# Kernel optimization log

Measured on AMD Instinct MI355X. Metric: run time of the kernel, lower is better.

Reference implementation:

```python
import jax, jax.numpy as jnp
import numpy as np

B, S, D, H = 2, 2048, 2048, 16
HD = D // H  # head_dim = 128
ROPE_BASE = 10000.0


def _rope_interleaved(x, cos, sin):
    # x: [B, S, H, HD]; cos/sin: [S, HD//2]
    xe = x[..., 0::2]
    xo = x[..., 1::2]
    c = cos[None, :, None, :]
    s = sin[None, :, None, :]
    oe = xe * c - xo * s
    oo = xe * s + xo * c
    # re-interleave pairs back to last dim
    return jnp.stack([oe, oo], axis=-1).reshape(x.shape)


def setup_inputs() -> dict:
    key = jax.random.key(0)
    k0, k1, k2, k3 = jax.random.split(key, 4)
    scale = D ** -0.5
    x = jax.random.normal(k0, (B, S, D), dtype=jnp.float32)
    wqk = jax.random.normal(k1, (2 * D, D), dtype=jnp.float32) * scale
    wv = jax.random.normal(k2, (D, D), dtype=jnp.float32) * scale
    wo = jax.random.normal(k3, (D, D), dtype=jnp.float32) * scale
    return {"x": x, "wqk": wqk, "wv": wv, "wo": wo}


def reference(x, wqk, wv, wo):
    b, s, d = x.shape
    # fused QK projection -> [B, S, 2, H, HD]
    xqk = (x @ wqk.T).reshape(b, s, 2, H, HD)
    xq = xqk[:, :, 0]
    xk = xqk[:, :, 1]
    xv = (x @ wv.T).reshape(b, s, H, HD)

    # interleaved rotary embedding (seqlen_offset=0, no-cache path)
    inv_freq = 1.0 / (ROPE_BASE ** (jnp.arange(0, HD, 2, dtype=jnp.float32) / HD))
    freqs = jnp.arange(s, dtype=jnp.float32)[:, None] * inv_freq[None, :]  # [S, HD//2]
    cos, sin = jnp.cos(freqs), jnp.sin(freqs)
    xq = _rope_interleaved(xq, cos, sin)
    xk = _rope_interleaved(xk, cos, sin)

    # causal scaled-dot-product attention
    scores = jnp.einsum("bqhd,bkhd->bhqk", xq, xk) * (HD ** -0.5)
    causal = jnp.tril(jnp.ones((s, s), dtype=bool))
    scores = jnp.where(causal[None, None], scores, jnp.finfo(scores.dtype).min)
    probs = jax.nn.softmax(scores, axis=-1)
    out = jnp.einsum("bhqk,bkhd->bqhd", probs, xv).reshape(b, s, d)
    return out @ wo.T
```

## Files before the change

kernel.cpp:

```cpp
#include <hip/hip_runtime.h>
#include <hip/hip_bf16.h>

#define NB 2
#define SEQ 2048
#define DMODEL 2048
#define NH 16
#define HD 128
#define QSCALE (0.08838834764831845f * 1.44269504088896f)
#define THRL2 11.5f

using bf16x8 = __attribute__((ext_vector_type(8))) __bf16;
using f32x4  = __attribute__((ext_vector_type(4))) float;

#define MFMA16 __builtin_amdgcn_mfma_f32_16x16x32_bf16

typedef __attribute__((address_space(1))) const void* gptr_t;
typedef __attribute__((address_space(3))) void* lptr_t;

__device__ inline void gload_lds16(const unsigned short* g, unsigned short* l) {
    __builtin_amdgcn_global_load_lds((gptr_t)g, (lptr_t)l, 16, 0, 0);
}

__device__ inline unsigned short f2b(float f) {
    unsigned u = __builtin_bit_cast(unsigned, f);
    u += 0x7FFF + ((u >> 16) & 1);
    return (unsigned short)(u >> 16);
}
__device__ inline float b2f(unsigned short h) {
    return __builtin_bit_cast(float, (unsigned)h << 16);
}
__device__ inline float fexp2(float x) {
    float r;
    asm("v_exp_f32 %0, %1" : "=v"(r) : "v"(x));
    return r;
}
__device__ inline unsigned cvtpk(float a, float b) {
    unsigned r;
    asm("v_cvt_pk_bf16_f32 %0, %1, %2" : "=v"(r) : "v"(a), "v"(b));
    return r;
}

__global__ void cast_all(const float* __restrict__ x, const float* __restrict__ wqk,
                         const float* __restrict__ wv, const float* __restrict__ wo,
                         unsigned short* __restrict__ xb, unsigned short* __restrict__ wb,
                         float2* __restrict__ tab) {
    int idx = blockIdx.x * 256 + threadIdx.x;
    if (idx < 6291456) {
        const float* src; unsigned short* dst; int off;
        if (idx < 2097152)      { src = x;   dst = xb;             off = 0; }
        else if (idx < 4194304) { src = wqk; dst = wb;             off = 2097152; }
        else if (idx < 5242880) { src = wv;  dst = wb + 8388608;   off = 4194304; }
        else                    { src = wo;  dst = wb + 12582912;  off = 5242880; }
        int i = (idx - off) * 4;
        float4 v = *reinterpret_cast<const float4*>(src + i);
        ushort4 o;
        o.x = f2b(v.x); o.y = f2b(v.y); o.z = f2b(v.z); o.w = f2b(v.w);
        *reinterpret_cast<ushort4*>(dst + i) = o;
    } else {
        int k = idx - 6291456;
        int i = k & 63;
        int s = k >> 6;
        float inv = exp2f(-13.287712379549449f * (float)i * (1.0f / 64.0f));
        float ang = (float)s * inv;
        float sn, cs;
        sincosf(ang, &sn, &cs);
        tab[k] = make_float2(cs, sn);
    }
}

template<int MODE>
__global__ __launch_bounds__(512) void gemm8p(const unsigned short* __restrict__ A,
                                              const unsigned short* __restrict__ Bw,
                                              void* __restrict__ Cout,
                                              unsigned short* __restrict__ qb,
                                              unsigned short* __restrict__ kbp,
                                              unsigned short* __restrict__ vx,
                                              const float2* __restrict__ tab,
                                              int M, int N, int K) {
    __shared__ __align__(16) char lds[98304];
    int tid = threadIdx.x;
    int lane = tid & 63;
    int wid = tid >> 6;
    int wm = wid >> 2, wn = wid & 3;
    int row0 = blockIdx.y * 128;
    int col0 = blockIdx.x * 256;
    int lr = lane & 15, g = lane >> 4;

    const unsigned short* srcA[2];
    const unsigned short* srcB[4];
#pragma unroll
    for (int i = 0; i < 2; i++) {
        int chunk = i * 512 + tid;
        int ksub = chunk >> 9;
        int cw = chunk & 511;
        int row = cw >> 2, c = cw & 3;
        int cs = c ^ ((row >> 1) & 3);
        srcA[i] = A + (size_t)(row0 + row) * K + ksub * 32 + cs * 8;
    }
#pragma unroll
    for (int i = 0; i < 4; i++) {
        int chunk = i * 512 + tid;
        int ksub = chunk >> 10;
        int cw = chunk & 1023;
        int row = cw >> 2, c = cw & 3;
        int cs = c ^ ((row >> 1) & 3);
        srcB[i] = Bw + (size_t)(col0 + row) * K + ksub * 32 + cs * 8;
    }

    int offA[4][2], offB[4][2];
#pragma unroll
    for (int i = 0; i < 4; i++) {
        int row = wm * 64 + i * 16 + lr;
#pragma unroll
        for (int ks = 0; ks < 2; ks++)
            offA[i][ks] = ks * 8192 + row * 64 + ((g ^ ((row >> 1) & 3)) * 16);
    }
#pragma unroll
    for (int j = 0; j < 4; j++) {
        int row = wn * 64 + j * 16 + lr;
#pragma unroll
        for (int ks = 0; ks < 2; ks++)
            offB[j][ks] = ks * 16384 + row * 64 + ((g ^ ((row >> 1) & 3)) * 16);
    }

    f32x4 acc[4][4] = {};
    int NT = K >> 6;

#define STAGE8(t) {                                                                   \
        int kb_ = (t) * 64;                                                           \
        int bs_ = ((t) & 1) * 49152;                                                  \
        _Pragma("unroll")                                                             \
        for (int i_ = 0; i_ < 2; i_++)                                                \
            gload_lds16(srcA[i_] + kb_,                                               \
                (unsigned short*)(lds + bs_ + (i_ * 512 + (tid & ~63)) * 16));        \
        _Pragma("unroll")                                                             \
        for (int i_ = 0; i_ < 4; i_++)                                                \
            gload_lds16(srcB[i_] + kb_,                                               \
                (unsigned short*)(lds + bs_ + 16384 + (i_ * 512 + (tid & ~63)) * 16)); \
    }

    STAGE8(0);
    for (int t = 0; t < NT; ++t) {
        if (t + 1 < NT) {
            STAGE8(t + 1);
            asm volatile("s_waitcnt vmcnt(6)" ::: "memory");
        } else {
            asm volatile("s_waitcnt vmcnt(0)" ::: "memory");
        }
        __builtin_amdgcn_s_barrier();
        __builtin_amdgcn_sched_barrier(0);

        const char* ab = lds + (t & 1) * 49152;
        const char* bb = ab + 16384;

        bf16x8 b[4][2], a[2][2];
#pragma unroll
        for (int j = 0; j < 4; j++)
#pragma unroll
            for (int ks = 0; ks < 2; ks++)
                b[j][ks] = *reinterpret_cast<const bf16x8*>(bb + offB[j][ks]);
#pragma unroll
        for (int i = 0; i < 2; i++)
#pragma unroll
            for (int ks = 0; ks < 2; ks++)
                a[i][ks] = *reinterpret_cast<const bf16x8*>(ab + offA[i][ks]);
        asm volatile("s_waitcnt lgkmcnt(0)" ::: "memory");
        __builtin_amdgcn_sched_barrier(0);
        __builtin_amdgcn_s_setprio(1);
#pragma unroll
        for (int ks = 0; ks < 2; ks++)
#pragma unroll
            for (int i = 0; i < 2; i++)
#pragma unroll
                for (int j = 0; j < 4; j++)
                    acc[i][j] = MFMA16(a[i][ks], b[j][ks], acc[i][j], 0, 0, 0);
        __builtin_amdgcn_s_setprio(0);

        bf16x8 a2[2][2];
#pragma unroll
        for (int i = 0; i < 2; i++)
#pragma unroll
            for (int ks = 0; ks < 2; ks++)
                a2[i][ks] = *reinterpret_cast<const bf16x8*>(ab + offA[2 + i][ks]);
        asm volatile("s_waitcnt lgkmcnt(0)" ::: "memory");
        __builtin_amdgcn_sched_barrier(0);
        __builtin_amdgcn_s_barrier();
        __builtin_amdgcn_sched_barrier(0);
        __builtin_amdgcn_s_setprio(1);
#pragma unroll
        for (int ks = 0; ks < 2; ks++)
#pragma unroll
            for (int i = 0; i < 2; i++)
#pragma unroll
                for (int j = 0; j < 4; j++)
                    acc[2 + i][j] = MFMA16(a2[i][ks], b[j][ks], acc[2 + i][j], 0, 0, 0);
        __builtin_amdgcn_s_setprio(0);
    }
#undef STAGE8

    int orow = g * 4;
    if (MODE == 0) {
#pragma unroll
        for (int i = 0; i < 4; i++) {
#pragma unroll
            for (int j = 0; j < 4; j++) {
                int r0 = row0 + wm * 64 + i * 16 + orow;
                int c  = col0 + wn * 64 + j * 16 + lr;
#pragma unroll
                for (int r = 0; r < 4; r++)
                    ((float*)Cout)[(size_t)(r0 + r) * N + c] = acc[i][j][r];
            }
        }
    } else {
        int bx = blockIdx.x;
        if (bx < 16) {
            const bool isQ = (bx < 8);
            unsigned short* dst = isQ ? qb : kbp;
#pragma unroll
            for (int i = 0; i < 4; i++) {
#pragma unroll
                for (int j = 0; j < 4; j++) {
                    int c = col0 + wn * 64 + j * 16 + lr;
                    int cc = c & 2047;
                    int h = cc >> 7, d = cc & 127, i2 = d >> 1;
                    int odd = lr & 1;
#pragma unroll
                    for (int r = 0; r < 4; r++) {
                        int trow = row0 + wm * 64 + i * 16 + orow + r;
                        int s = trow & (SEQ - 1), bb2 = trow >> 11;
                        float v = acc[i][j][r];
                        float pv = __shfl_xor(v, 1);
                        float2 cssn = tab[s * 64 + i2];
                        float out = odd ? (pv * cssn.y + v * cssn.x)
                                        : (v * cssn.x - pv * cssn.y);
                        if (isQ) out *= QSCALE;
                        dst[((size_t)((bb2 * NH + h) * SEQ + s)) * HD + d] = f2b(out);
                    }
                }
            }
        } else {
#pragma unroll
            for (int i = 0; i < 4; i++) {
#pragma unroll
                for (int j = 0; j < 4; j++) {
                    int cc = col0 + wn * 64 + j * 16 + lr - 4096;
#pragma unroll
                    for (int r = 0; r < 4; r++) {
                        int trow = row0 + wm * 64 + i * 16 + orow + r;
                        vx[(size_t)trow * 2048 + cc] = f2b(acc[i][j][r]);
                    }
                }
            }
        }
    }
}

__global__ __launch_bounds__(256) void v_tr(const unsigned short* __restrict__ vx,
                                            unsigned short* __restrict__ vt) {
    __shared__ unsigned short tl[64][68];
    int bid = blockIdx.x;
    int st = bid & 31;
    int dt = (bid >> 5) & 1;
    int bh = bid >> 6;
    int b = bh >> 4, h = bh & 15;
    int tid = threadIdx.x;
    int rr = tid >> 2;
    int rc = (tid & 3) * 16;

    const unsigned short* src = vx + (size_t)(b * SEQ + st * 64 + rr) * 2048 + h * HD + dt * 64 + rc;
    uint4 v0 = *reinterpret_cast<const uint4*>(src);
    uint4 v1 = *reinterpret_cast<const uint4*>(src + 8);
    *reinterpret_cast<uint4*>(&tl[rr][rc]) = v0;
    *reinterpret_cast<uint4*>(&tl[rr][rc + 8]) = v1;
    __syncthreads();

    unsigned short tmp[16];
#pragma unroll
    for (int k = 0; k < 16; k++) tmp[k] = tl[rc + k][rr];
    unsigned short* dst = vt + (size_t)(bh * HD + dt * 64 + rr) * SEQ + st * 64 + rc;
    *reinterpret_cast<uint4*>(dst)     = *reinterpret_cast<const uint4*>(&tmp[0]);
    *reinterpret_cast<uint4*>(dst + 8) = *reinterpret_cast<const uint4*>(&tmp[8]);
}

__global__ __launch_bounds__(64, 2) void attn8(const unsigned short* __restrict__ Q,
                                               const unsigned short* __restrict__ Kb,
                                               const unsigned short* __restrict__ Vt,
                                               unsigned short* __restrict__ O) {
    __shared__ __align__(16) char lds[18432];

    int lane = threadIdx.x;
    int bid = blockIdx.x;
    int qt = 63 - (bid >> 5);
    int bh = bid & 31;
    int q0 = qt * 32;
    int ktiles = qt + 1;
    int lr = lane & 15;
    int g  = lane >> 4;
    int g4 = g * 4;
    int lk = g * 8;

    const unsigned short* Qp = Q  + (size_t)bh * SEQ * HD;
    const unsigned short* Kp = Kb + (size_t)bh * SEQ * HD;
    const unsigned short* Vp = Vt + (size_t)bh * HD * SEQ;
    char* pl = lds + 16384;
    int b = bh >> 4;
    int h = bh & 15;

    int srcoff[8];
#pragma unroll
    for (int i2 = 0; i2 < 8; ++i2) {
        int r = i2 * 4 + g;
        srcoff[i2] = r * HD + ((lr ^ (r & 7)) * 8);
    }

#define STAGEK32(bufbase, kvbase)                                                   \
    {                                                                               \
        const unsigned short* kbase = Kp + (size_t)(kvbase) * HD;                   \
        _Pragma("unroll")                                                           \
        for (int i2 = 0; i2 < 8; ++i2)                                              \
            gload_lds16(kbase + srcoff[i2],                                         \
                        (unsigned short*)(lds + (bufbase) + i2 * 1024));            \
    }

    bf16x8 qf[2][4];
#pragma unroll
    for (int f = 0; f < 2; f++)
#pragma unroll
        for (int kb = 0; kb < 4; kb++)
            qf[f][kb] = *reinterpret_cast<const bf16x8*>(Qp + (size_t)(q0 + f * 16 + lr) * HD + kb * 32 + lk);

    f32x4 oacc[2][8] = {};
    float m[2] = { -1e30f, -1e30f }, l[2] = { 0.0f, 0.0f };
    int qrow[2] = { q0 + lr, q0 + 16 + lr };

    STAGEK32(0, 0);

    int cur = 0;
    for (int t = 0; t < ktiles; ++t) {
        int kv0 = t * 32;
        if (t + 1 < ktiles) {
            STAGEK32((cur ^ 1) * 8192, kv0 + 32);
            asm volatile("s_waitcnt vmcnt(8)" ::: "memory");
        } else {
            asm volatile("s_waitcnt vmcnt(0)" ::: "memory");
        }
        __builtin_amdgcn_sched_barrier(0);

        char* kb_c = lds + cur * 8192;
        f32x4 s[2][2] = {};
#pragma unroll
        for (int kb = 0; kb < 4; kb++) {
#pragma unroll
            for (int jj = 0; jj < 2; jj++) {
                int row = jj * 16 + lr;
                int cin = ((kb * 4 + g) ^ (row & 7));
                bf16x8 kf = *reinterpret_cast<const bf16x8*>(kb_c + row * 256 + cin * 16);
                s[0][jj] = MFMA16(kf, qf[0][kb], s[0][jj], 0, 0, 0);
                s[1][jj] = MFMA16(kf, qf[1][kb], s[1][jj], 0, 0, 0);
            }
        }

        bf16x8 vf[8];
#pragma unroll
        for (int db = 0; db < 8; db++)
            vf[db] = *reinterpret_cast<const bf16x8*>(Vp + (size_t)(db * 16 + lr) * SEQ + kv0 + lk);

#pragma unroll
        for (int f = 0; f < 2; f++) {
            int q = qrow[f];
            bool full = (kv0 + 31 <= q0 + f * 16);
            float mx = -1e30f;
            if (full) {
#pragma unroll
                for (int jj = 0; jj < 2; jj++)
#pragma unroll
                    for (int r = 0; r < 4; r++)
                        mx = fmaxf(mx, s[f][jj][r]);
            } else {
#pragma unroll
                for (int jj = 0; jj < 2; jj++)
#pragma unroll
                    for (int r = 0; r < 4; r++) {
                        int kv = kv0 + jj * 16 + g4 + r;
                        float v = (kv <= q) ? s[f][jj][r] : -1e30f;
                        s[f][jj][r] = v;
                        mx = fmaxf(mx, v);
                    }
            }
            mx = fmaxf(mx, __shfl_xor(mx, 16));
            mx = fmaxf(mx, __shfl_xor(mx, 32));

            if (!__all(mx <= m[f] + THRL2)) {
                float mn = fmaxf(m[f], mx);
                float sc = fexp2(m[f] - mn);
                m[f] = mn;
                l[f] *= sc;
#pragma unroll
                for (int db = 0; db < 8; db++)
#pragma unroll
                    for (int r = 0; r < 4; r++)
                        oacc[f][db][r] *= sc;
            }

            int row = f * 16 + lr;
            int rb = row * 64;
            int sw = (row & 3) << 4;
            float rs = 0.0f;
#pragma unroll
            for (int jj = 0; jj < 2; jj++)
#pragma unroll
                for (int hh = 0; hh < 2; hh++) {
                    float p0 = fexp2(s[f][jj][2 * hh]     - m[f]);
                    float p1 = fexp2(s[f][jj][2 * hh + 1] - m[f]);
                    rs += p0 + p1;
                    unsigned pk = cvtpk(p0, p1);
                    int colb = jj * 32 + g * 8 + 4 * hh;
                    *reinterpret_cast<unsigned*>(pl + rb + (colb ^ sw)) = pk;
                }
            rs += __shfl_xor(rs, 16);
            rs += __shfl_xor(rs, 32);
            l[f] += rs;
        }

        asm volatile("s_waitcnt lgkmcnt(0)" ::: "memory");
        __builtin_amdgcn_sched_barrier(0);

        bf16x8 pb[2];
#pragma unroll
        for (int f = 0; f < 2; f++) {
            int row = f * 16 + lr;
            int off = row * 64 + ((g * 16) ^ ((row & 3) << 4));
            pb[f] = *reinterpret_cast<const bf16x8*>(pl + off);
        }
#pragma unroll
        for (int db = 0; db < 8; db++) {
            oacc[0][db] = MFMA16(vf[db], pb[0], oacc[0][db], 0, 0, 0);
            oacc[1][db] = MFMA16(vf[db], pb[1], oacc[1][db], 0, 0, 0);
        }

        cur ^= 1;
    }

#pragma unroll
    for (int f = 0; f < 2; f++) {
        float inv = 1.0f / l[f];
        int q = q0 + f * 16 + lr;
        unsigned short* op = O + ((size_t)(b * SEQ + q)) * DMODEL + h * HD;
#pragma unroll
        for (int db = 0; db < 8; db++) {
            ushort4 o4;
            o4.x = f2b(oacc[f][db][0] * inv);
            o4.y = f2b(oacc[f][db][1] * inv);
            o4.z = f2b(oacc[f][db][2] * inv);
            o4.w = f2b(oacc[f][db][3] * inv);
            *reinterpret_cast<ushort4*>(op + db * 16 + g4) = o4;
        }
    }
#undef STAGEK32
}

extern "C" void kernel_launch(void* const* d_in, const int* in_sizes, int n_in,
                              void* d_out, int out_size, void* d_ws, size_t ws_size,
                              hipStream_t stream) {
    const float* x   = (const float*)d_in[0];
    const float* wqk = (const float*)d_in[1];
    const float* wv  = (const float*)d_in[2];
    const float* wo  = (const float*)d_in[3];

    unsigned short* xb  = (unsigned short*)d_ws;
    unsigned short* wb  = xb  + (size_t)8388608;
    unsigned short* qb  = wb  + (size_t)16777216;
    unsigned short* kb  = qb  + (size_t)8388608;
    unsigned short* vx  = kb  + (size_t)8388608;
    unsigned short* vt  = vx  + (size_t)8388608;
    unsigned short* ao  = vt  + (size_t)8388608;
    float2* tab = (float2*)(ao + (size_t)8388608);

    cast_all<<<25088, 256, 0, stream>>>(x, wqk, wv, wo, xb, wb, tab);

    gemm8p<2><<<dim3(24, 32), 512, 0, stream>>>(xb, wb, nullptr, qb, kb, vx, tab, 4096, 6144, 2048);

    v_tr<<<2048, 256, 0, stream>>>(vx, vt);

    attn8<<<2048, 64, 0, stream>>>(qb, kb, vt, ao);

    gemm8p<0><<<dim3(8, 32), 512, 0, stream>>>(ao, wb + 12582912, d_out, nullptr, nullptr, nullptr, nullptr, 4096, 2048, 2048);
}
```

Measured before the change: 279.5 us.

## Use 256x256-tile QKV GEMM and write V transposed directly from epilogue

Replaces the 128x256-tile QKV projection GEMM with a new 256x256-tile kernel that uses 128 KB of LDS, double-buffered with direct global-to-LDS loads, giving more operand reuse per tile. Its V epilogue writes the transposed bf16 layout directly, so the separate v_tr transpose kernel and the intermediate vx buffer are removed. The output projection GEMM is simplified to a non-templated version. The trade-offs are fewer blocks (384) across the GPU, which may cause wave-quantization or occupancy loss, and less coalesced strided ushort4 stores for V.

```diff
diff --git a/kernel.cpp b/kernel.cpp
--- a/kernel.cpp
+++ b/kernel.cpp
@@ -68,14 +68,188 @@
     }
 }
 
-template<int MODE>
+__global__ __launch_bounds__(512) void gemm256(const unsigned short* __restrict__ A,
+                                               const unsigned short* __restrict__ Bw,
+                                               unsigned short* __restrict__ qb,
+                                               unsigned short* __restrict__ kbp,
+                                               unsigned short* __restrict__ vt,
+                                               const float2* __restrict__ tab,
+                                               int M, int N, int K) {
+    __shared__ __align__(16) char lds[131072];
+    int tid = threadIdx.x;
+    int lane = tid & 63;
+    int wid = tid >> 6;
+    int wm = wid >> 2, wn = wid & 3;
+    int row0 = blockIdx.y * 256;
+    int col0 = blockIdx.x * 256;
+    int lr = lane & 15, g = lane >> 4;
+
+    const unsigned short* srcA[4];
+    const unsigned short* srcB[4];
+#pragma unroll
+    for (int i = 0; i < 4; i++) {
+        int chunk = i * 512 + tid;
+        int ksub = chunk >> 10;
+        int cw = chunk & 1023;
+        int row = cw >> 2, c = cw & 3;
+        int cs = c ^ ((row >> 1) & 3);
+        srcA[i] = A  + (size_t)(row0 + row) * K + ksub * 32 + cs * 8;
+        srcB[i] = Bw + (size_t)(col0 + row) * K + ksub * 32 + cs * 8;
+    }
+
+    int offA[8][2], offB[4][2];
+#pragma unroll
+    for (int i = 0; i < 8; i++) {
+        int row = wm * 128 + i * 16 + lr;
+#pragma unroll
+        for (int ks = 0; ks < 2; ks++)
+            offA[i][ks] = ks * 16384 + row * 64 + ((g ^ ((row >> 1) & 3)) * 16);
+    }
+#pragma unroll
+    for (int j = 0; j < 4; j++) {
+        int row = wn * 64 + j * 16 + lr;
+#pragma unroll
+        for (int ks = 0; ks < 2; ks++)
+            offB[j][ks] = 32768 + ks * 16384 + row * 64 + ((g ^ ((row >> 1) & 3)) * 16);
+    }
+
+    f32x4 acc[8][4] = {};
+    int NT = K >> 6;
+
+#define STAGE256(t) {                                                                 \
+        int kb_ = (t) * 64;                                                           \
+        int bs_ = ((t) & 1) * 65536;                                                  \
+        _Pragma("unroll")                                                             \
+        for (int i_ = 0; i_ < 4; i_++)                                                \
+            gload_lds16(srcA[i_] + kb_,                                               \
+                (unsigned short*)(lds + bs_ + (i_ * 512 + (tid & ~63)) * 16));        \
+        _Pragma("unroll")                                                             \
+        for (int i_ = 0; i_ < 4; i_++)                                                \
+            gload_lds16(srcB[i_] + kb_,                                               \
+                (unsigned short*)(lds + bs_ + 32768 + (i_ * 512 + (tid & ~63)) * 16)); \
+    }
+
+    STAGE256(0);
+    for (int t = 0; t < NT; ++t) {
+        if (t + 1 < NT) {
+            STAGE256(t + 1);
+            asm volatile("s_waitcnt vmcnt(8)" ::: "memory");
+        } else {
+            asm volatile("s_waitcnt vmcnt(0)" ::: "memory");
+        }
+        __builtin_amdgcn_s_barrier();
+        __builtin_amdgcn_sched_barrier(0);
+
+        const char* bufc = lds + (t & 1) * 65536;
+        bf16x8 av[4], bv[4];
+
+#pragma unroll
+        for (int j = 0; j < 4; j++) bv[j] = *reinterpret_cast<const bf16x8*>(bufc + offB[j][0]);
+#pragma unroll
+        for (int i = 0; i < 4; i++) av[i] = *reinterpret_cast<const bf16x8*>(bufc + offA[i][0]);
+        asm volatile("s_waitcnt lgkmcnt(0)" ::: "memory");
+        __builtin_amdgcn_sched_barrier(0);
+        __builtin_amdgcn_s_setprio(1);
+#pragma unroll
+        for (int i = 0; i < 4; i++)
+#pragma unroll
+            for (int j = 0; j < 4; j++)
+                acc[i][j] = MFMA16(av[i], bv[j], acc[i][j], 0, 0, 0);
+        __builtin_amdgcn_s_setprio(0);
+
+#pragma unroll
+        for (int i = 0; i < 4; i++) av[i] = *reinterpret_cast<const bf16x8*>(bufc + offA[4 + i][0]);
+        asm volatile("s_waitcnt lgkmcnt(0)" ::: "memory");
+        __builtin_amdgcn_sched_barrier(0);
+        __builtin_amdgcn_s_setprio(1);
+#pragma unroll
+        for (int i = 0; i < 4; i++)
+#pragma unroll
+            for (int j = 0; j < 4; j++)
+                acc[4 + i][j] = MFMA16(av[i], bv[j], acc[4 + i][j], 0, 0, 0);
+        __builtin_amdgcn_s_setprio(0);
+
+#pragma unroll
+        for (int j = 0; j < 4; j++) bv[j] = *reinterpret_cast<const bf16x8*>(bufc + offB[j][1]);
+#pragma unroll
+        for (int i = 0; i < 4; i++) av[i] = *reinterpret_cast<const bf16x8*>(bufc + offA[i][1]);
+        asm volatile("s_waitcnt lgkmcnt(0)" ::: "memory");
+        __builtin_amdgcn_sched_barrier(0);
+        __builtin_amdgcn_s_setprio(1);
+#pragma unroll
+        for (int i = 0; i < 4; i++)
+#pragma unroll
+            for (int j = 0; j < 4; j++)
+                acc[i][j] = MFMA16(av[i], bv[j], acc[i][j], 0, 0, 0);
+        __builtin_amdgcn_s_setprio(0);
+
+#pragma unroll
+        for (int i = 0; i < 4; i++) av[i] = *reinterpret_cast<const bf16x8*>(bufc + offA[4 + i][1]);
+        asm volatile("s_waitcnt lgkmcnt(0)" ::: "memory");
+        __builtin_amdgcn_sched_barrier(0);
+        __builtin_amdgcn_s_barrier();
+        __builtin_amdgcn_sched_barrier(0);
+        __builtin_amdgcn_s_setprio(1);
+#pragma unroll
+        for (int i = 0; i < 4; i++)
+#pragma unroll
+            for (int j = 0; j < 4; j++)
+                acc[4 + i][j] = MFMA16(av[i], bv[j], acc[4 + i][j], 0, 0, 0);
+        __builtin_amdgcn_s_setprio(0);
+    }
+#undef STAGE256
+
+    int orow = g * 4;
+    int bx = blockIdx.x;
+    if (bx < 16) {
+        const bool isQ = (bx < 8);
+        unsigned short* dst = isQ ? qb : kbp;
+#pragma unroll
+        for (int i = 0; i < 8; i++) {
+#pragma unroll
+            for (int j = 0; j < 4; j++) {
+                int c = col0 + wn * 64 + j * 16 + lr;
+                int cc = c & 2047;
+                int h = cc >> 7, d = cc & 127, i2 = d >> 1;
+                int odd = lr & 1;
+#pragma unroll
+                for (int r = 0; r < 4; r++) {
+                    int trow = row0 + wm * 128 + i * 16 + orow + r;
+                    int s = trow & (SEQ - 1), bb2 = trow >> 11;
+                    float v = acc[i][j][r];
+                    float pv = __shfl_xor(v, 1);
+                    float2 cssn = tab[s * 64 + i2];
+                    float out = odd ? (pv * cssn.y + v * cssn.x)
+                                    : (v * cssn.x - pv * cssn.y);
+                    if (isQ) out *= QSCALE;
+                    dst[((size_t)((bb2 * NH + h) * SEQ + s)) * HD + d] = f2b(out);
+                }
+            }
+        }
+    } else {
+#pragma unroll
+        for (int i = 0; i < 8; i++) {
+#pragma unroll
+            for (int j = 0; j < 4; j++) {
+                int cc = col0 + wn * 64 + j * 16 + lr - 4096;
+                int h = cc >> 7, d = cc & 127;
+                int trow0 = row0 + wm * 128 + i * 16 + orow;
+                int s0 = trow0 & (SEQ - 1), bb2 = trow0 >> 11;
+                int bh = bb2 * NH + h;
+                ushort4 o4;
+                o4.x = f2b(acc[i][j][0]);
+                o4.y = f2b(acc[i][j][1]);
+                o4.z = f2b(acc[i][j][2]);
+                o4.w = f2b(acc[i][j][3]);
+                *reinterpret_cast<ushort4*>(vt + ((size_t)bh * HD + d) * SEQ + s0) = o4;
+            }
+        }
+    }
+}
+
 __global__ __launch_bounds__(512) void gemm8p(const unsigned short* __restrict__ A,
                                               const unsigned short* __restrict__ Bw,
-                                              void* __restrict__ Cout,
-                                              unsigned short* __restrict__ qb,
-                                              unsigned short* __restrict__ kbp,
-                                              unsigned short* __restrict__ vx,
-                                              const float2* __restrict__ tab,
+                                              float* __restrict__ Cout,
                                               int M, int N, int K) {
     __shared__ __align__(16) char lds[98304];
     int tid = threadIdx.x;
@@ -199,87 +373,17 @@
 #undef STAGE8
 
     int orow = g * 4;
-    if (MODE == 0) {
-#pragma unroll
-        for (int i = 0; i < 4; i++) {
-#pragma unroll
-            for (int j = 0; j < 4; j++) {
-                int r0 = row0 + wm * 64 + i * 16 + orow;
-                int c  = col0 + wn * 64 + j * 16 + lr;
-#pragma unroll
-                for (int r = 0; r < 4; r++)
-                    ((float*)Cout)[(size_t)(r0 + r) * N + c] = acc[i][j][r];
-            }
-        }
-    } else {
-        int bx = blockIdx.x;
-        if (bx < 16) {
-            const bool isQ = (bx < 8);
-            unsigned short* dst = isQ ? qb : kbp;
-#pragma unroll
-            for (int i = 0; i < 4; i++) {
-#pragma unroll
-                for (int j = 0; j < 4; j++) {
-                    int c = col0 + wn * 64 + j * 16 + lr;
-                    int cc = c & 2047;
-                    int h = cc >> 7, d = cc & 127, i2 = d >> 1;
-                    int odd = lr & 1;
-#pragma unroll
-                    for (int r = 0; r < 4; r++) {
-                        int trow = row0 + wm * 64 + i * 16 + orow + r;
-                        int s = trow & (SEQ - 1), bb2 = trow >> 11;
-                        float v = acc[i][j][r];
-                        float pv = __shfl_xor(v, 1);
-                        float2 cssn = tab[s * 64 + i2];
-                        float out = odd ? (pv * cssn.y + v * cssn.x)
-                                        : (v * cssn.x - pv * cssn.y);
-                        if (isQ) out *= QSCALE;
-                        dst[((size_t)((bb2 * NH + h) * SEQ + s)) * HD + d] = f2b(out);
-                    }
-                }
-            }
-        } else {
-#pragma unroll
-            for (int i = 0; i < 4; i++) {
-#pragma unroll
-                for (int j = 0; j < 4; j++) {
-                    int cc = col0 + wn * 64 + j * 16 + lr - 4096;
-#pragma unroll
-                    for (int r = 0; r < 4; r++) {
-                        int trow = row0 + wm * 64 + i * 16 + orow + r;
-                        vx[(size_t)trow * 2048 + cc] = f2b(acc[i][j][r]);
-                    }
-                }
-            }
-        }
-    }
-}
-
-__global__ __launch_bounds__(256) void v_tr(const unsigned short* __restrict__ vx,
-                                            unsigned short* __restrict__ vt) {
-    __shared__ unsigned short tl[64][68];
-    int bid = blockIdx.x;
-    int st = bid & 31;
-    int dt = (bid >> 5) & 1;
-    int bh = bid >> 6;
-    int b = bh >> 4, h = bh & 15;
-    int tid = threadIdx.x;
-    int rr = tid >> 2;
-    int rc = (tid & 3) * 16;
-
-    const unsigned short* src = vx + (size_t)(b * SEQ + st * 64 + rr) * 2048 + h * HD + dt * 64 + rc;
-    uint4 v0 = *reinterpret_cast<const uint4*>(src);
-    uint4 v1 = *reinterpret_cast<const uint4*>(src + 8);
-    *reinterpret_cast<uint4*>(&tl[rr][rc]) = v0;
-    *reinterpret_cast<uint4*>(&tl[rr][rc + 8]) = v1;
-    __syncthreads();
-
-    unsigned short tmp[16];
-#pragma unroll
-    for (int k = 0; k < 16; k++) tmp[k] = tl[rc + k][rr];
-    unsigned short* dst = vt + (size_t)(bh * HD + dt * 64 + rr) * SEQ + st * 64 + rc;
-    *reinterpret_cast<uint4*>(dst)     = *reinterpret_cast<const uint4*>(&tmp[0]);
-    *reinterpret_cast<uint4*>(dst + 8) = *reinterpret_cast<const uint4*>(&tmp[8]);
+#pragma unroll
+    for (int i = 0; i < 4; i++) {
+#pragma unroll
+        for (int j = 0; j < 4; j++) {
+            int r0 = row0 + wm * 64 + i * 16 + orow;
+            int c  = col0 + wn * 64 + j * 16 + lr;
+#pragma unroll
+            for (int r = 0; r < 4; r++)
+                Cout[(size_t)(r0 + r) * N + c] = acc[i][j][r];
+        }
+    }
 }
 
 __global__ __launch_bounds__(64, 2) void attn8(const unsigned short* __restrict__ Q,
@@ -471,18 +575,15 @@
     unsigned short* wb  = xb  + (size_t)8388608;
     unsigned short* qb  = wb  + (size_t)16777216;
     unsigned short* kb  = qb  + (size_t)8388608;
-    unsigned short* vx  = kb  + (size_t)8388608;
-    unsigned short* vt  = vx  + (size_t)8388608;
+    unsigned short* vt  = kb  + (size_t)8388608;
     unsigned short* ao  = vt  + (size_t)8388608;
     float2* tab = (float2*)(ao + (size_t)8388608);
 
     cast_all<<<25088, 256, 0, stream>>>(x, wqk, wv, wo, xb, wb, tab);
 
-    gemm8p<2><<<dim3(24, 32), 512, 0, stream>>>(xb, wb, nullptr, qb, kb, vx, tab, 4096, 6144, 2048);
-
-    v_tr<<<2048, 256, 0, stream>>>(vx, vt);
+    gemm256<<<dim3(24, 16), 512, 0, stream>>>(xb, wb, qb, kb, vt, tab, 4096, 6144, 2048);
 
     attn8<<<2048, 64, 0, stream>>>(qb, kb, vt, ao);
 
-    gemm8p<0><<<dim3(8, 32), 512, 0, stream>>>(ao, wb + 12582912, d_out, nullptr, nullptr, nullptr, nullptr, 4096, 2048, 2048);
-}
+    gemm8p<<<dim3(8, 32), 512, 0, stream>>>(ao, wb + 12582912, d_out ? (float*)d_out : nullptr, 4096, 2048, 2048);
+}
```

Result: slower. 291.0 us (+4.1%).
